# Performance work log

Measured on AMD Instinct MI355X. Metric: run time of the kernel, lower is better.

The kernel has to match this reference:

```python
import jax, jax.numpy as jnp
import numpy as np
from functools import partial

N_NODES = 100000
N_EDGES = 1600000
N_LABEL = 200000
D = 128


def _add_self_loops(edge_index, edge_weight, num_nodes):
    # PyG GCNConv default: add self loops with fill_value = 1.0
    loops = jnp.arange(num_nodes, dtype=edge_index.dtype)
    src = jnp.concatenate([edge_index[0], loops])
    dst = jnp.concatenate([edge_index[1], loops])
    ew = jnp.concatenate([edge_weight, jnp.ones((num_nodes,), edge_weight.dtype)])
    return src, dst, ew


def _gcn_norm(src, dst, ew, num_nodes):
    # symmetric normalization: D^-1/2 A D^-1/2, degrees over target index
    deg = jax.ops.segment_sum(ew, dst, num_segments=num_nodes)
    dinv = jnp.where(deg > 0, jax.lax.rsqrt(deg), 0.0)
    return dinv[src] * ew * dinv[dst]


def _gcn_conv(x, W, b, src, dst, norm, num_nodes):
    h = x @ W                      # [N, D] small GEMM
    msg = h[src] * norm[:, None]   # gather + scale, [E+N, D]
    out = jax.ops.segment_sum(msg, dst, num_segments=num_nodes)
    return out + b


def setup_inputs() -> dict:
    key = jax.random.key(0)
    ks = jax.random.split(key, 10)
    s = 1.0 / np.sqrt(D)
    return {
        "x": jax.random.normal(ks[0], (N_NODES, D), jnp.float32),
        "edge_index": jax.random.randint(ks[1], (2, N_EDGES), 0, N_NODES, jnp.int64),
        "edge_weight": jax.random.uniform(ks[2], (N_EDGES,), jnp.float32),
        "edge_label_index": jax.random.randint(ks[3], (2, N_LABEL), 0, N_NODES, jnp.int64),
        "W1": jax.random.uniform(ks[4], (D, D), jnp.float32, -s, s),
        "b1": jnp.zeros((D,), jnp.float32),
        "W2": jax.random.uniform(ks[5], (D, D), jnp.float32, -s, s),
        "b2": jnp.zeros((D,), jnp.float32),
        "lin_W": jax.random.uniform(ks[6], (D, D), jnp.float32, -s, s),
        "lin_b": jax.random.uniform(ks[7], (D,), jnp.float32, -s, s),
    }


def reference(x, edge_index, edge_weight, edge_label_index, W1, b1, W2, b2, lin_W, lin_b):
    n = x.shape[0]
    src, dst, ew = _add_self_loops(edge_index, edge_weight, n)
    norm = _gcn_norm(src, dst, ew, n)
    out = jax.nn.relu(_gcn_conv(x, W1, b1, src, dst, norm, n))
    out = jax.nn.relu(_gcn_conv(out, W2, b2, src, dst, norm, n))
    had = out[edge_label_index[0]] * out[edge_label_index[1]]  # [EL, D]
    # lin then sum over features == had @ lin_W @ 1 + sum(lin_b)
    return jnp.sum(had @ lin_W + lin_b, axis=-1)
```

## Files before the change

### kernel.cpp

```cpp
#include <hip/hip_runtime.h>

#define N_NODES 100000
#define N_EDGES 1600000
#define N_LABEL 200000
#define D 128

#define SCAN_BLOCKS ((N_NODES + 255) / 256)

typedef __attribute__((ext_vector_type(8))) short short8;
typedef __attribute__((ext_vector_type(4))) float f32x4;

static __device__ __forceinline__ unsigned short f2bf(float f) {
    unsigned u = __float_as_uint(f);
    u += 0x7fffu + ((u >> 16) & 1u);
    return (unsigned short)(u >> 16);
}
static __device__ __forceinline__ float bf2f_lo(unsigned p) {
    return __uint_as_float(p << 16);
}
static __device__ __forceinline__ float bf2f_hi(unsigned p) {
    return __uint_as_float(p & 0xffff0000u);
}

__global__ void k_prepall(const float* __restrict__ linW, const float* __restrict__ linb,
                          const float* __restrict__ W1, const float* __restrict__ W2,
                          float* __restrict__ wv, float* __restrict__ cval,
                          unsigned short* __restrict__ w1t,
                          unsigned short* __restrict__ w2t) {
    int b = blockIdx.x;
    if (b == 0) {
        int t = threadIdx.x;
        if (t < 128) {
            float s = 0.f;
            for (int j = 0; j < D; ++j) s += linW[t * D + j];
            wv[t] = s;
        }
        __shared__ float red[128];
        if (t < 128) red[t] = linb[t];
        __syncthreads();
        for (int st = 64; st > 0; st >>= 1) {
            if (t < st) red[t] += red[t + st];
            __syncthreads();
        }
        if (t == 0) *cval = red[0];
    } else if (b <= 64) {
        int i = (b - 1) * 256 + threadIdx.x;
        int k = i >> 7, n = i & 127;
        w1t[n * D + k] = f2bf(W1[i]);
    } else {
        int i = (b - 65) * 256 + threadIdx.x;
        int k = i >> 7, n = i & 127;
        w2t[n * D + k] = f2bf(W2[i]);
    }
}

__global__ void k_init(int* __restrict__ cnt8) {
    int i = blockIdx.x * 256 + threadIdx.x;
    if (i < 8 * N_NODES) cnt8[i] = 0;
}

__global__ void k_count(const int* __restrict__ ei, int* __restrict__ cnt8,
                        int* __restrict__ rank) {
    int e = blockIdx.x * 256 + threadIdx.x;
    int p = blockIdx.x & 7;
    if (e < N_EDGES) rank[e] = atomicAdd(&cnt8[p * N_NODES + ei[N_EDGES + e]], 1);
}

__global__ void k_scan1(const int* __restrict__ cnt8, int* __restrict__ offs,
                        int* __restrict__ bsum) {
    __shared__ int sm[256];
    int tid = threadIdx.x;
    int i = blockIdx.x * 256 + tid;
    int v = 0;
    if (i < N_NODES) {
#pragma unroll
        for (int q = 0; q < 8; ++q) v += cnt8[q * N_NODES + i];
    }
    sm[tid] = v;
    __syncthreads();
    for (int st = 1; st < 256; st <<= 1) {
        int add = (tid >= st) ? sm[tid - st] : 0;
        __syncthreads();
        sm[tid] += add;
        __syncthreads();
    }
    if (i < N_NODES) offs[i] = sm[tid] - v;
    if (tid == 255) bsum[blockIdx.x] = sm[255];
}

__global__ void k_scan2(int* __restrict__ bsum) {
    __shared__ int sm[512];
    int tid = threadIdx.x;
    int v = (tid < SCAN_BLOCKS) ? bsum[tid] : 0;
    sm[tid] = v;
    __syncthreads();
    for (int st = 1; st < 512; st <<= 1) {
        int add = (tid >= st) ? sm[tid - st] : 0;
        __syncthreads();
        sm[tid] += add;
        __syncthreads();
    }
    if (tid < SCAN_BLOCKS) bsum[tid] = sm[tid] - v;
}

__global__ void k_scan3(int* __restrict__ offs, const int* __restrict__ bsum,
                        const int* __restrict__ cnt8, int* __restrict__ pofs) {
    int i = blockIdx.x * 256 + threadIdx.x;
    if (i < N_NODES) {
        int base = offs[i] + bsum[i >> 8];
        offs[i] = base;
#pragma unroll
        for (int q = 0; q < 8; ++q) {
            pofs[q * N_NODES + i] = base;
            base += cnt8[q * N_NODES + i];
        }
    }
    if (i == 0) offs[N_NODES] = N_EDGES;
}

__global__ void k_scatter(const int* __restrict__ ei, const float* __restrict__ ew,
                          const int* __restrict__ pofs, const int* __restrict__ rank,
                          int2* __restrict__ csr) {
    int e = blockIdx.x * 256 + threadIdx.x;
    int p = blockIdx.x & 7;
    if (e < N_EDGES) {
        int d = ei[N_EDGES + e];
        int pos = pofs[p * N_NODES + d] + rank[e];
        csr[pos] = make_int2(ei[e] << 6, __float_as_int(ew[e]));
    }
}

__global__ void k_degdinv(const int* __restrict__ offs, const int2* __restrict__ csr,
                          float* __restrict__ dinv) {
    int i = blockIdx.x * 256 + threadIdx.x;
    if (i < N_NODES) {
        int p0 = offs[i], p1 = offs[i + 1];
        float s = 1.0f;
        for (int p = p0; p < p1; ++p) s += __int_as_float(csr[p].y);
        dinv[i] = rsqrtf(s);
    }
}

template <bool IN_F32>
__global__ __launch_bounds__(256) void k_gemm(const void* __restrict__ INp,
                                              const unsigned short* __restrict__ Wt,
                                              const float* __restrict__ dinv,
                                              unsigned short* __restrict__ H) {
    __shared__ unsigned short xs[64 * 128];
    __shared__ unsigned short wts[128 * 128];
    int tid = threadIdx.x;
    int rowBase = blockIdx.x * 64;

#pragma unroll
    for (int i = 0; i < 4; ++i) {
        int idx = tid + i * 256;
        int r = idx >> 4;
        int kc = (idx & 15) << 3;
        int gr = rowBase + r;
        uint4 pk = make_uint4(0, 0, 0, 0);
        if (gr < N_NODES) {
            if (IN_F32) {
                const float* X = (const float*)INp;
                float4 v0 = *(const float4*)&X[(size_t)gr * D + kc];
                float4 v1 = *(const float4*)&X[(size_t)gr * D + kc + 4];
                pk.x = (unsigned)f2bf(v0.x) | ((unsigned)f2bf(v0.y) << 16);
                pk.y = (unsigned)f2bf(v0.z) | ((unsigned)f2bf(v0.w) << 16);
                pk.z = (unsigned)f2bf(v1.x) | ((unsigned)f2bf(v1.y) << 16);
                pk.w = (unsigned)f2bf(v1.z) | ((unsigned)f2bf(v1.w) << 16);
            } else {
                pk = *(const uint4*)&((const unsigned short*)INp)[(size_t)gr * D + kc];
            }
        }
        *(uint4*)&xs[(r * D + kc) ^ ((r & 7) << 3)] = pk;
    }
#pragma unroll
    for (int i = 0; i < 8; ++i) {
        int idx = tid + i * 256;
        int n = idx >> 4;
        int kc = (idx & 15) << 3;
        uint4 pk = *(const uint4*)&Wt[n * D + kc];
        *(uint4*)&wts[(n * D + kc) ^ ((n & 7) << 3)] = pk;
    }
    __syncthreads();

    int lane = tid & 63;
    int wrow = (tid >> 6) * 16;
    int l15 = lane & 15;
    int l4 = (lane >> 4) << 2;

    f32x4 acc[8] = {};
    union FragU { short8 v; uint2 u2[2]; };

#pragma unroll
    for (int kk = 0; kk < 4; ++kk) {
        int kb = kk * 32 + l4;
        int m = wrow + l15;
        FragU a;
        a.u2[0] = *(uint2*)&xs[(m * D + kb) ^ ((m & 7) << 3)];
        a.u2[1] = *(uint2*)&xs[(m * D + kb + 16) ^ ((m & 7) << 3)];
#pragma unroll
        for (int ct = 0; ct < 8; ++ct) {
            int n = ct * 16 + l15;
            FragU b;
            b.u2[0] = *(uint2*)&wts[(n * D + kb) ^ ((n & 7) << 3)];
            b.u2[1] = *(uint2*)&wts[(n * D + kb + 16) ^ ((n & 7) << 3)];
            acc[ct] = __builtin_amdgcn_mfma_f32_16x16x32_bf16(a.v, b.v, acc[ct], 0, 0, 0);
        }
    }

    int rloc = wrow + l4;
    float dn[4];
#pragma unroll
    for (int r = 0; r < 4; ++r) {
        int gr = rowBase + rloc + r;
        dn[r] = (gr < N_NODES) ? dinv[gr] : 0.f;
    }
#pragma unroll
    for (int ct = 0; ct < 8; ++ct) {
#pragma unroll
        for (int r = 0; r < 4; ++r) {
            int gr = rowBase + rloc + r;
            if (gr < N_NODES)
                H[(size_t)gr * D + ct * 16 + l15] = f2bf(acc[ct][r] * dn[r]);
        }
    }
}

__global__ __launch_bounds__(256) void k_agg(const unsigned* __restrict__ h,
                                             const float* __restrict__ dinv,
                                             const int* __restrict__ offs,
                                             const int2* __restrict__ csr,
                                             const float* __restrict__ bias,
                                             unsigned* __restrict__ out) {
    int wid = threadIdx.x >> 6;
    int lane = threadIdx.x & 63;
    int node = blockIdx.x * 4 + wid;
    if (node >= N_NODES) return;

    int eh = lane >> 5;
    int fl = lane & 31;

    float a0 = 0.f, a1 = 0.f, a2 = 0.f, a3 = 0.f;
    int p0 = offs[node], p1 = offs[node + 1];

    for (int p = p0; p < p1; p += 16) {
        int2 cc[8];
        float ww[8];
#pragma unroll
        for (int k = 0; k < 8; ++k) {
            int pe = p + (k << 1) + eh;
            bool v = pe < p1;
            cc[k] = csr[v ? pe : p0];
            ww[k] = v ? __int_as_float(cc[k].y) : 0.f;
        }
        uint2 hh[8];
#pragma unroll
        for (int k = 0; k < 8; ++k)
            hh[k] = *(const uint2*)&h[(size_t)(unsigned)cc[k].x + fl * 2];
#pragma unroll
        for (int k = 0; k < 8; ++k) {
            a0 += ww[k] * bf2f_lo(hh[k].x);
            a1 += ww[k] * bf2f_hi(hh[k].x);
            a2 += ww[k] * bf2f_lo(hh[k].y);
            a3 += ww[k] * bf2f_hi(hh[k].y);
        }
    }

    a0 += __shfl_xor(a0, 32, 64);
    a1 += __shfl_xor(a1, 32, 64);
    a2 += __shfl_xor(a2, 32, 64);
    a3 += __shfl_xor(a3, 32, 64);

    if (eh == 0) {
        uint2 sv = *(const uint2*)&h[(size_t)node * 64 + fl * 2];
        a0 += bf2f_lo(sv.x);
        a1 += bf2f_hi(sv.x);
        a2 += bf2f_lo(sv.y);
        a3 += bf2f_hi(sv.y);
        float dn = dinv[node];
        float4 bb = *(const float4*)&bias[fl * 4];
        a0 = fmaxf(a0 * dn + bb.x, 0.f);
        a1 = fmaxf(a1 * dn + bb.y, 0.f);
        a2 = fmaxf(a2 * dn + bb.z, 0.f);
        a3 = fmaxf(a3 * dn + bb.w, 0.f);
        uint2 o;
        o.x = (unsigned)f2bf(a0) | ((unsigned)f2bf(a1) << 16);
        o.y = (unsigned)f2bf(a2) | ((unsigned)f2bf(a3) << 16);
        *(uint2*)&out[(size_t)node * 64 + fl * 2] = o;
    }
}

__global__ void k_final(const int* __restrict__ eli, const unsigned* __restrict__ o2,
                        const float* __restrict__ wv, const float* __restrict__ cval,
                        float* __restrict__ res) {
    unsigned g = blockIdx.x * 256 + threadIdx.x;
    int l = g >> 6;
    int t = g & 63;
    if (l < N_LABEL) {
        int a = eli[l];
        int b = eli[N_LABEL + l];
        unsigned ua = o2[(size_t)a * 64 + t];
        unsigned ub = o2[(size_t)b * 64 + t];
        float2 w2 = *(const float2*)&wv[t * 2];
        float s = bf2f_lo(ua) * bf2f_lo(ub) * w2.x + bf2f_hi(ua) * bf2f_hi(ub) * w2.y;
#pragma unroll
        for (int st = 32; st > 0; st >>= 1) s += __shfl_down(s, st, 64);
        if (t == 0) res[l] = s + *cval;
    }
}

extern "C" void kernel_launch(void* const* d_in, const int* in_sizes, int n_in,
                              void* d_out, int out_size, void* d_ws, size_t ws_size,
                              hipStream_t stream) {
    const float* x    = (const float*)d_in[0];
    const int*   ei   = (const int*)d_in[1];
    const float* ew   = (const float*)d_in[2];
    const int*   eli  = (const int*)d_in[3];
    const float* W1   = (const float*)d_in[4];
    const float* b1   = (const float*)d_in[5];
    const float* W2   = (const float*)d_in[6];
    const float* b2   = (const float*)d_in[7];
    const float* linW = (const float*)d_in[8];
    const float* linb = (const float*)d_in[9];
    float* res = (float*)d_out;

    float*          ws    = (float*)d_ws;
    float*          dinv  = ws;
    int*            offs  = (int*)(dinv + N_NODES);
    int*            bsum  = offs + N_NODES + 4;
    int*            cnt8  = bsum + 512;
    int*            pofs  = cnt8 + 8 * N_NODES;
    int2*           csr   = (int2*)(pofs + 8 * N_NODES);
    unsigned*       h_bf  = (unsigned*)(csr + N_EDGES);
    unsigned*       agg   = h_bf + (size_t)N_NODES * 64;
    unsigned*       out2  = agg + (size_t)N_NODES * 64;
    float*          wv    = (float*)(out2 + (size_t)N_NODES * 64);
    float*          cval  = wv + D;
    unsigned short* w1t   = (unsigned short*)(cval + 1);
    unsigned short* w2t   = w1t + D * D;
    int*            rank  = (int*)agg;

    k_prepall<<<129, 256, 0, stream>>>(linW, linb, W1, W2, wv, cval, w1t, w2t);

    k_init<<<(8 * N_NODES + 255) / 256, 256, 0, stream>>>(cnt8);
    k_count<<<(N_EDGES + 255) / 256, 256, 0, stream>>>(ei, cnt8, rank);
    k_scan1<<<SCAN_BLOCKS, 256, 0, stream>>>(cnt8, offs, bsum);
    k_scan2<<<1, 512, 0, stream>>>(bsum);
    k_scan3<<<SCAN_BLOCKS, 256, 0, stream>>>(offs, bsum, cnt8, pofs);
    k_scatter<<<(N_EDGES + 255) / 256, 256, 0, stream>>>(ei, ew, pofs, rank, csr);
    k_degdinv<<<(N_NODES + 255) / 256, 256, 0, stream>>>(offs, csr, dinv);

    const int GB = (N_NODES + 63) / 64;

    k_gemm<true><<<GB, 256, 0, stream>>>(x, w1t, dinv, (unsigned short*)h_bf);
    k_agg<<<(N_NODES + 3) / 4, 256, 0, stream>>>(h_bf, dinv, offs, csr, b1, agg);

    k_gemm<false><<<GB, 256, 0, stream>>>(agg, w2t, dinv, (unsigned short*)h_bf);
    k_agg<<<(N_NODES + 3) / 4, 256, 0, stream>>>(h_bf, dinv, offs, csr, b2, out2);

    k_final<<<(N_LABEL * 64 + 255) / 256, 256, 0, stream>>>(eli, out2, wv, cval, res);
}
```

Before: 368.2 us.

## Fold cnt8 init into prep kernel, restructure agg and final, nontemporal stores

```diff
diff --git a/kernel.cpp b/kernel.cpp
--- a/kernel.cpp
+++ b/kernel.cpp
@@ -26,7 +26,8 @@
                           const float* __restrict__ W1, const float* __restrict__ W2,
                           float* __restrict__ wv, float* __restrict__ cval,
                           unsigned short* __restrict__ w1t,
-                          unsigned short* __restrict__ w2t) {
+                          unsigned short* __restrict__ w2t,
+                          int* __restrict__ cnt8) {
     int b = blockIdx.x;
     if (b == 0) {
         int t = threadIdx.x;
@@ -47,23 +48,24 @@
         int i = (b - 1) * 256 + threadIdx.x;
         int k = i >> 7, n = i & 127;
         w1t[n * D + k] = f2bf(W1[i]);
-    } else {
+    } else if (b <= 128) {
         int i = (b - 65) * 256 + threadIdx.x;
         int k = i >> 7, n = i & 127;
         w2t[n * D + k] = f2bf(W2[i]);
-    }
-}
-
-__global__ void k_init(int* __restrict__ cnt8) {
-    int i = blockIdx.x * 256 + threadIdx.x;
-    if (i < 8 * N_NODES) cnt8[i] = 0;
+    } else {
+        int i = (b - 129) * 256 + threadIdx.x;
+        if (i < 8 * N_NODES) cnt8[i] = 0;
+    }
 }
 
 __global__ void k_count(const int* __restrict__ ei, int* __restrict__ cnt8,
                         int* __restrict__ rank) {
     int e = blockIdx.x * 256 + threadIdx.x;
     int p = blockIdx.x & 7;
-    if (e < N_EDGES) rank[e] = atomicAdd(&cnt8[p * N_NODES + ei[N_EDGES + e]], 1);
+    if (e < N_EDGES) {
+        int r = atomicAdd(&cnt8[p * N_NODES + ei[N_EDGES + e]], 1);
+        __builtin_nontemporal_store(r, &rank[e]);
+    }
 }
 
 __global__ void k_scan1(const int* __restrict__ cnt8, int* __restrict__ offs,
@@ -126,7 +128,9 @@
     if (e < N_EDGES) {
         int d = ei[N_EDGES + e];
         int pos = pofs[p * N_NODES + d] + rank[e];
-        csr[pos] = make_int2(ei[e] << 6, __float_as_int(ew[e]));
+        long long rec = (unsigned)(ei[e] << 6) |
+                        ((long long)(unsigned)__float_as_int(ew[e]) << 32);
+        __builtin_nontemporal_store(rec, (long long*)&csr[pos]);
     }
 }
 
@@ -232,79 +236,62 @@
                                              const int2* __restrict__ csr,
                                              const float* __restrict__ bias,
                                              unsigned* __restrict__ out) {
-    int wid = threadIdx.x >> 6;
     int lane = threadIdx.x & 63;
-    int node = blockIdx.x * 4 + wid;
+    int node = __builtin_amdgcn_readfirstlane(blockIdx.x * 4 + (threadIdx.x >> 6));
     if (node >= N_NODES) return;
 
-    int eh = lane >> 5;
-    int fl = lane & 31;
-
-    float a0 = 0.f, a1 = 0.f, a2 = 0.f, a3 = 0.f;
     int p0 = offs[node], p1 = offs[node + 1];
-
-    for (int p = p0; p < p1; p += 16) {
+    float a0 = 0.f, a1 = 0.f;
+
+    for (int p = p0; p < p1; p += 8) {
         int2 cc[8];
         float ww[8];
 #pragma unroll
         for (int k = 0; k < 8; ++k) {
-            int pe = p + (k << 1) + eh;
+            int pe = p + k;
             bool v = pe < p1;
             cc[k] = csr[v ? pe : p0];
             ww[k] = v ? __int_as_float(cc[k].y) : 0.f;
         }
-        uint2 hh[8];
+        unsigned hh[8];
 #pragma unroll
         for (int k = 0; k < 8; ++k)
-            hh[k] = *(const uint2*)&h[(size_t)(unsigned)cc[k].x + fl * 2];
+            hh[k] = h[(size_t)(unsigned)cc[k].x + lane];
 #pragma unroll
         for (int k = 0; k < 8; ++k) {
-            a0 += ww[k] * bf2f_lo(hh[k].x);
-            a1 += ww[k] * bf2f_hi(hh[k].x);
-            a2 += ww[k] * bf2f_lo(hh[k].y);
-            a3 += ww[k] * bf2f_hi(hh[k].y);
-        }
-    }
-
-    a0 += __shfl_xor(a0, 32, 64);
-    a1 += __shfl_xor(a1, 32, 64);
-    a2 += __shfl_xor(a2, 32, 64);
-    a3 += __shfl_xor(a3, 32, 64);
-
-    if (eh == 0) {
-        uint2 sv = *(const uint2*)&h[(size_t)node * 64 + fl * 2];
-        a0 += bf2f_lo(sv.x);
-        a1 += bf2f_hi(sv.x);
-        a2 += bf2f_lo(sv.y);
-        a3 += bf2f_hi(sv.y);
-        float dn = dinv[node];
-        float4 bb = *(const float4*)&bias[fl * 4];
-        a0 = fmaxf(a0 * dn + bb.x, 0.f);
-        a1 = fmaxf(a1 * dn + bb.y, 0.f);
-        a2 = fmaxf(a2 * dn + bb.z, 0.f);
-        a3 = fmaxf(a3 * dn + bb.w, 0.f);
-        uint2 o;
-        o.x = (unsigned)f2bf(a0) | ((unsigned)f2bf(a1) << 16);
-        o.y = (unsigned)f2bf(a2) | ((unsigned)f2bf(a3) << 16);
-        *(uint2*)&out[(size_t)node * 64 + fl * 2] = o;
-    }
+            a0 += ww[k] * bf2f_lo(hh[k]);
+            a1 += ww[k] * bf2f_hi(hh[k]);
+        }
+    }
+
+    unsigned sv = h[(size_t)node * 64 + lane];
+    a0 += bf2f_lo(sv);
+    a1 += bf2f_hi(sv);
+    float dn = dinv[node];
+    float2 bb = *(const float2*)&bias[lane * 2];
+    a0 = fmaxf(a0 * dn + bb.x, 0.f);
+    a1 = fmaxf(a1 * dn + bb.y, 0.f);
+    out[(size_t)node * 64 + lane] = (unsigned)f2bf(a0) | ((unsigned)f2bf(a1) << 16);
 }
 
 __global__ void k_final(const int* __restrict__ eli, const unsigned* __restrict__ o2,
                         const float* __restrict__ wv, const float* __restrict__ cval,
                         float* __restrict__ res) {
     unsigned g = blockIdx.x * 256 + threadIdx.x;
-    int l = g >> 6;
-    int t = g & 63;
+    int l = g >> 5;
+    int t = g & 31;
     if (l < N_LABEL) {
         int a = eli[l];
         int b = eli[N_LABEL + l];
-        unsigned ua = o2[(size_t)a * 64 + t];
-        unsigned ub = o2[(size_t)b * 64 + t];
-        float2 w2 = *(const float2*)&wv[t * 2];
-        float s = bf2f_lo(ua) * bf2f_lo(ub) * w2.x + bf2f_hi(ua) * bf2f_hi(ub) * w2.y;
-#pragma unroll
-        for (int st = 32; st > 0; st >>= 1) s += __shfl_down(s, st, 64);
+        uint2 ua = *(const uint2*)&o2[(size_t)a * 64 + t * 2];
+        uint2 ub = *(const uint2*)&o2[(size_t)b * 64 + t * 2];
+        float4 w4 = *(const float4*)&wv[t * 4];
+        float s = bf2f_lo(ua.x) * bf2f_lo(ub.x) * w4.x
+                + bf2f_hi(ua.x) * bf2f_hi(ub.x) * w4.y
+                + bf2f_lo(ua.y) * bf2f_lo(ub.y) * w4.z
+                + bf2f_hi(ua.y) * bf2f_hi(ub.y) * w4.w;
+#pragma unroll
+        for (int st = 16; st > 0; st >>= 1) s += __shfl_down(s, st, 32);
         if (t == 0) res[l] = s + *cval;
     }
 }
@@ -340,9 +327,9 @@
     unsigned short* w2t   = w1t + D * D;
     int*            rank  = (int*)agg;
 
-    k_prepall<<<129, 256, 0, stream>>>(linW, linb, W1, W2, wv, cval, w1t, w2t);
-
-    k_init<<<(8 * N_NODES + 255) / 256, 256, 0, stream>>>(cnt8);
+    k_prepall<<<129 + (8 * N_NODES + 255) / 256, 256, 0, stream>>>(
+        linW, linb, W1, W2, wv, cval, w1t, w2t, cnt8);
+
     k_count<<<(N_EDGES + 255) / 256, 256, 0, stream>>>(ei, cnt8, rank);
     k_scan1<<<SCAN_BLOCKS, 256, 0, stream>>>(cnt8, offs, bsum);
     k_scan2<<<1, 512, 0, stream>>>(bsum);
@@ -358,5 +345,5 @@
     k_gemm<false><<<GB, 256, 0, stream>>>(agg, w2t, dinv, (unsigned short*)h_bf);
     k_agg<<<(N_NODES + 3) / 4, 256, 0, stream>>>(h_bf, dinv, offs, csr, b2, out2);
 
-    k_final<<<(N_LABEL * 64 + 255) / 256, 256, 0, stream>>>(eli, out2, wv, cval, res);
-}
+    k_final<<<(N_LABEL * 32 + 255) / 256, 256, 0, stream>>>(eli, out2, wv, cval, res);
+}
```

After: 380.8 us. 3.4% more time.
